# Optimization experiments

Hardware: AMD Instinct MI355X
Metric: run time of the kernel (lower is better)

The kernel has to match this reference:

```python
import jax, jax.numpy as jnp
import numpy as np

B, T, HID = 2, 2048, 2048
N_HEADS, N_KV, HEAD_DIM = 32, 8, 64
THETA = 10000.0
SCALE = HEAD_DIM ** -0.5
STEPS = 2  # entries already in cache before this call (step_idx)


def _rope_cos_sin(pos):
    # pos: [B, T] int -> cos/sin [B, T, HEAD_DIM]
    inv_freq = 1.0 / (THETA ** (jnp.arange(0, HEAD_DIM, 2, dtype=jnp.float32) / HEAD_DIM))
    freqs = pos.astype(jnp.float32)[..., None] * inv_freq  # [B,T,D/2]
    emb = jnp.concatenate([freqs, freqs], axis=-1)
    return jnp.cos(emb), jnp.sin(emb)


def _rotate_half(x):
    x1, x2 = jnp.split(x, 2, axis=-1)
    return jnp.concatenate([-x2, x1], axis=-1)


def setup_inputs() -> dict:
    key = jax.random.key(0)
    ks = jax.random.split(key, 8)
    combined_states = jax.random.normal(ks[0], (B, T, 2 * HID), dtype=jnp.float32)
    # additive causal mask: 0 on/below diagonal, large negative above
    causal = jnp.tril(jnp.ones((T, T), dtype=bool))
    attention_mask = jnp.where(causal, 0.0, -1e9).astype(jnp.float32)[None, None].repeat(B, axis=0)
    position_ids = jnp.broadcast_to(jnp.arange(T, dtype=jnp.int32), (B, T))
    prev_k = jax.random.normal(ks[1], (STEPS, B, N_HEADS, T, HEAD_DIM), dtype=jnp.float32)
    prev_v = jax.random.normal(ks[2], (STEPS, B, N_HEADS, T, HEAD_DIM), dtype=jnp.float32)
    Wq = 0.02 * jax.random.normal(ks[3], (2 * HID, N_HEADS * HEAD_DIM), dtype=jnp.float32)
    Wk = 0.02 * jax.random.normal(ks[4], (2 * HID, N_KV * HEAD_DIM), dtype=jnp.float32)
    Wv = 0.02 * jax.random.normal(ks[5], (2 * HID, N_KV * HEAD_DIM), dtype=jnp.float32)
    Wo = 0.02 * jax.random.normal(ks[6], (N_HEADS * HEAD_DIM, HID), dtype=jnp.float32)
    return {"combined_states": combined_states, "attention_mask": attention_mask,
            "position_ids": position_ids, "prev_k": prev_k, "prev_v": prev_v,
            "Wq": Wq, "Wk": Wk, "Wv": Wv, "Wo": Wo}


def reference(combined_states, attention_mask, position_ids, prev_k, prev_v, Wq, Wk, Wv, Wo):
    b, t, _ = combined_states.shape
    step_idx = prev_k.shape[0]  # len(cache_k) before append
    groups = N_HEADS // N_KV

    # fused QKV projection -> [B, H, T, D]
    q = (combined_states @ Wq).reshape(b, t, N_HEADS, HEAD_DIM).transpose(0, 2, 1, 3)
    k = (combined_states @ Wk).reshape(b, t, N_KV, HEAD_DIM).transpose(0, 2, 1, 3)
    v = (combined_states @ Wv).reshape(b, t, N_KV, HEAD_DIM).transpose(0, 2, 1, 3)

    # RoPE with phase shift by step_idx
    cos, sin = _rope_cos_sin(position_ids + step_idx)
    cos, sin = cos[:, None], sin[:, None]  # [B,1,T,D]
    q = q * cos + _rotate_half(q) * sin
    k = k * cos + _rotate_half(k) * sin

    # GQA expansion (repeat_interleave over head dim)
    k = jnp.repeat(k, groups, axis=1)
    v = jnp.repeat(v, groups, axis=1)

    # cache after append: [prev_0, prev_1, ..., k_new]; k0 = cache[0], later = cache[1:]
    k0, v0 = prev_k[0], prev_v[0]
    later_k = jnp.concatenate([prev_k[1:], k[None]], axis=0)  # [S, B, H, T, D], S = step_idx
    later_v = jnp.concatenate([prev_v[1:], v[None]], axis=0)

    # block attention over K_0 plus growing diagonal terms
    attn = jnp.einsum('bhtd,bhsd->bhts', q, k0) * SCALE + attention_mask  # [B,H,T,T]
    diag = jnp.einsum('bhtd,sbhtd->bhts', q, later_k) * SCALE             # [B,H,T,S]
    logits = jnp.concatenate([attn, diag], axis=-1)                        # [B,H,T,T+S]
    probs = jax.nn.softmax(logits.astype(jnp.float32), axis=-1).astype(q.dtype)

    out = jnp.einsum('bhts,bhsd->bhtd', probs[..., :t], v0)
    out = out + jnp.einsum('bhts,sbhtd->bhtd', probs[..., t:], later_v)
    out = out.transpose(0, 2, 1, 3).reshape(b, t, N_HEADS * HEAD_DIM)
    return out @ Wo
```

## Files before the change

kernel.cpp:

```cpp
#include <hip/hip_runtime.h>

#define B_    2
#define T_    2048
#define HID_  2048
#define NH_   32
#define NKV_  8
#define HD_   64
#define STEPS_ 2
#define SCALE_ 0.125f
#define CSC_  0.18033688011112042f

typedef float   f32x4  __attribute__((ext_vector_type(4)));
typedef __bf16  bf16x8 __attribute__((ext_vector_type(8)));
typedef unsigned short u16x8 __attribute__((ext_vector_type(8)));

__device__ __forceinline__ unsigned short f2bf(float f) {
  unsigned int u = __builtin_bit_cast(unsigned int, f);
  u = (u + 0x7fffu + ((u >> 16) & 1u)) >> 16;
  return (unsigned short)u;
}
__device__ __forceinline__ float bf2f(unsigned short h) {
  unsigned int u = ((unsigned int)h) << 16;
  return __builtin_bit_cast(float, u);
}
__device__ __forceinline__ bf16x8 frag_ld(const unsigned short* p) {
  u16x8 v = *(const u16x8*)p;
  return __builtin_bit_cast(bf16x8, v);
}
__device__ __forceinline__ f32x4 mfma16(bf16x8 a, bf16x8 b, f32x4 c) {
  return __builtin_amdgcn_mfma_f32_16x16x32_bf16(a, b, c, 0, 0, 0);
}
__device__ __forceinline__ void async_cp16(const void* g, void* l) {
  __builtin_amdgcn_global_load_lds(
      (const __attribute__((address_space(1))) void*)g,
      (__attribute__((address_space(3))) void*)l, 16, 0, 0);
}
__device__ __forceinline__ unsigned int cvtpk_bf16(float lo, float hi) {
  unsigned int r;
  asm("v_cvt_pk_bf16_f32 %0, %1, %2" : "=v"(r) : "v"(lo), "v"(hi));
  return r;
}

__global__ __launch_bounds__(256) void preproc(const float* __restrict__ X,
                                               const float* __restrict__ prevk,
                                               const float* __restrict__ prevv,
                                               const float* __restrict__ Wq,
                                               const float* __restrict__ Wk,
                                               const float* __restrict__ Wv,
                                               const float* __restrict__ Wo,
                                               const int* __restrict__ pos_ids,
                                               unsigned short* __restrict__ Xb,
                                               unsigned short* __restrict__ k0b,
                                               unsigned short* __restrict__ WqkvT,
                                               unsigned short* __restrict__ WoT,
                                               unsigned short* __restrict__ v0t,
                                               float2* __restrict__ cstab) {
  __shared__ float tile[128][65];
  const int tid = threadIdx.x;
  int blk = blockIdx.x;

  if (blk < 16384) {
    int idx = blk * 256 + tid;
    float4 v = ((const float4*)X)[idx];
    ushort4 o;
    o.x = f2bf(v.x); o.y = f2bf(v.y); o.z = f2bf(v.z); o.w = f2bf(v.w);
    ((ushort4*)Xb)[idx] = o;
    return;
  }
  blk -= 16384;
  if (blk < 8192) {
    int idx = blk * 256 + tid;
    float4 v = ((const float4*)prevk)[idx];
    ushort4 o;
    o.x = f2bf(v.x); o.y = f2bf(v.y); o.z = f2bf(v.z); o.w = f2bf(v.w);
    ((ushort4*)k0b)[idx] = o;
    return;
  }
  blk -= 8192;
  if (blk < 512) {
    int idx = blk * 256 + tid;
    int i = idx & 31;
    int pos = pos_ids[idx >> 5] + STEPS_;
    float inv = exp2f(-(float)i * (13.287712379549449f / 32.0f));
    float ang = (float)pos * inv;
    float ss, cc;
    sincosf(ang, &ss, &cc);
    cstab[idx] = make_float2(cc, ss);
    return;
  }
  blk -= 512;

  const float* in;
  unsigned short* out;
  int N, ldo, k0, n0;
  if (blk < 1536) {
    int nt = blk % 48, kt = blk / 48;
    k0 = kt * 128;
    ldo = 4096;
    if (nt < 32)      { in = Wq; N = 2048; out = WqkvT;                         n0 = nt * 64; }
    else if (nt < 40) { in = Wk; N = 512;  out = WqkvT + (size_t)2048 * 4096;   n0 = (nt - 32) * 64; }
    else              { in = Wv; N = 512;  out = WqkvT + (size_t)2560 * 4096;   n0 = (nt - 40) * 64; }
  } else if (blk < 2048) {
    int q = blk - 1536;
    int nt = q % 32, kt = q / 32;
    in = Wo; out = WoT; N = 2048; ldo = 2048;
    k0 = kt * 128; n0 = nt * 64;
  } else {
    int q = blk - 2048;
    int st = q % 16, bh = q / 16;
    in = prevv + (size_t)bh * T_ * HD_;
    out = v0t + (size_t)bh * HD_ * T_;
    N = 64; ldo = T_;
    k0 = st * 128; n0 = 0;
  }

  const int c = tid & 63, w = tid >> 6;
#pragma unroll
  for (int i = 0; i < 32; i++) {
    int r = w * 32 + i;
    tile[r][c] = in[(size_t)(k0 + r) * N + n0 + c];
  }
  __syncthreads();
#pragma unroll
  for (int ii = 0; ii < 16; ii++) {
    int rr = w * 16 + ii;
    unsigned int u = (unsigned int)f2bf(tile[c * 2][rr]) |
                     ((unsigned int)f2bf(tile[c * 2 + 1][rr]) << 16);
    *(unsigned int*)&out[(size_t)(n0 + rr) * ldo + k0 + c * 2] = u;
  }
}

#define SBAR  do { __builtin_amdgcn_sched_barrier(0); __builtin_amdgcn_s_barrier(); \
                   __builtin_amdgcn_sched_barrier(0); } while (0)
#define LGKM0 do { asm volatile("s_waitcnt lgkmcnt(0)" ::: "memory"); \
                   __builtin_amdgcn_sched_barrier(0); } while (0)
#define VM2   do { asm volatile("s_waitcnt vmcnt(2)" ::: "memory"); } while (0)
#define VM0   do { asm volatile("s_waitcnt vmcnt(0)" ::: "memory"); } while (0)

template <int NF>
__global__ __launch_bounds__(512, 2) void gemm128_bt(const unsigned short* __restrict__ A,
                                                     const unsigned short* __restrict__ Bt,
                                                     float* __restrict__ C,
                                                     int M, int N, int K) {
  constexpr int NHF = NF / 2;
  constexpr int BROWS = 128 + NF * 64;
  __shared__ __attribute__((aligned(128))) unsigned short smem[2][BROWS * 64];

  const int tid  = threadIdx.x;
  const int lane = tid & 63;
  const int wid  = tid >> 6;
  const int wr   = wid >> 2;
  const int wc   = wid & 3;
  const int la   = lane & 15;
  const int lq   = lane >> 4;
  const int sw   = la & 7;
  const int m0   = blockIdx.x * 128;
  const int n0   = blockIdx.y * (NF * 64);

  const int sr = lane >> 3;
  const int sl = (lane & 7) ^ sr;

  const unsigned short* gA[2];
  const unsigned short* gB[NHF][2];
#pragma unroll
  for (int is = 0; is < 2; ++is) {
    int r = (wid * 2 + is) * 8 + sr;
    gA[is] = A + (size_t)(m0 + r) * K + sl * 8;
#pragma unroll
    for (int u = 0; u < NHF; ++u)
      gB[u][is] = Bt + (size_t)(n0 + u * 128 + r) * K + sl * 8;
  }

#define G_STG_A(buf, kt) do { \
    async_cp16(gA[0] + (size_t)(kt) * 64, &smem[buf][(wid * 2 + 0) * 512]); \
    async_cp16(gA[1] + (size_t)(kt) * 64, &smem[buf][(wid * 2 + 1) * 512]); \
  } while (0)
#define G_STG_B(buf, u, kt) do { \
    async_cp16(gB[u][0] + (size_t)(kt) * 64, &smem[buf][(128 + (u) * 128) * 64 + (wid * 2 + 0) * 512]); \
    async_cp16(gB[u][1] + (size_t)(kt) * 64, &smem[buf][(128 + (u) * 128) * 64 + (wid * 2 + 1) * 512]); \
  } while (0)

  f32x4  acc[4][NF] = {};
  bf16x8 aR[2][2], b0r[NHF][2], b1r[NHF][2];

#define G_RD_A(buf, qm) do { \
    const unsigned short* rp_ = &smem[buf][0]; \
    _Pragma("unroll") \
    for (int i_ = 0; i_ < 2; ++i_) { \
      int ro_ = (wr * 64 + (qm) * 32 + i_ * 16 + la) * 64; \
      aR[i_][0] = frag_ld(rp_ + ro_ + (((0 + lq) ^ sw) << 3)); \
      aR[i_][1] = frag_ld(rp_ + ro_ + (((4 + lq) ^ sw) << 3)); \
    } \
  } while (0)
#define G_RD_B(buf, qn, breg) do { \
    const unsigned short* rp_ = &smem[buf][128 * 64]; \
    _Pragma("unroll") \
    for (int j_ = 0; j_ < NHF; ++j_) { \
      int ro_ = (wc * (NF * 16) + (qn) * (NF * 8) + j_ * 16 + la) * 64; \
      breg[j_][0] = frag_ld(rp_ + ro_ + (((0 + lq) ^ sw) << 3)); \
      breg[j_][1] = frag_ld(rp_ + ro_ + (((4 + lq) ^ sw) << 3)); \
    } \
  } while (0)
#define G_MMA(qm, qn, breg) do { \
    _Pragma("unroll") \
    for (int i_ = 0; i_ < 2; ++i_) \
      _Pragma("unroll") \
      for (int j_ = 0; j_ < NHF; ++j_) { \
        f32x4 c_ = acc[(qm) * 2 + i_][(qn) * NHF + j_]; \
        c_ = mfma16(aR[i_][0], breg[j_][0], c_); \
        c_ = mfma16(aR[i_][1], breg[j_][1], c_); \
        acc[(qm) * 2 + i_][(qn) * NHF + j_] = c_; \
      } \
  } while (0)

  G_STG_A(0, 0);
#pragma unroll
  for (int u = 0; u < NHF; ++u) G_STG_B(0, u, 0);
  if constexpr (NF == 6) G_STG_B(1, 2, 1); else G_STG_A(1, 1);
  VM2;
  SBAR;

  const int NI = K >> 7;
  for (int it = 0; it < NI; ++it) {
    const int e = it * 2;
    const bool pf = (it + 1 < NI);
    G_RD_A(0, 0);
    G_RD_B(0, 0, b0r);
    if constexpr (NF == 6) G_STG_A(1, e + 1); else G_STG_B(1, 0, e + 1);
    SBAR; LGKM0;
    __builtin_amdgcn_s_setprio(1); G_MMA(0, 0, b0r); __builtin_amdgcn_s_setprio(0);
    SBAR;
    G_RD_B(0, 1, b1r);
    if constexpr (NF == 6) G_STG_B(1, 0, e + 1); else G_STG_B(1, 1, e + 1);
    SBAR; LGKM0;
    __builtin_amdgcn_s_setprio(1); G_MMA(0, 1, b1r); __builtin_amdgcn_s_setprio(0);
    SBAR;
    G_RD_A(0, 1);
    if constexpr (NF == 6) G_STG_B(1, 1, e + 1);
    SBAR; LGKM0;
    __builtin_amdgcn_s_setprio(1); G_MMA(1, 1, b1r); __builtin_amdgcn_s_setprio(0);
    SBAR;
    if (pf) G_STG_A(0, e + 2);
    SBAR; LGKM0;
    __builtin_amdgcn_s_setprio(1); G_MMA(1, 0, b0r); __builtin_amdgcn_s_setprio(0);
    if (pf) { VM2; } else { VM0; }
    SBAR;
    G_RD_A(1, 0);
    G_RD_B(1, 0, b0r);
    if (pf) G_STG_B(0, 0, e + 2);
    SBAR; LGKM0;
    __builtin_amdgcn_s_setprio(1); G_MMA(0, 0, b0r); __builtin_amdgcn_s_setprio(0);
    SBAR;
    G_RD_B(1, 1, b1r);
    if (pf) G_STG_B(0, 1, e + 2);
    SBAR; LGKM0;
    __builtin_amdgcn_s_setprio(1); G_MMA(0, 1, b1r); __builtin_amdgcn_s_setprio(0);
    SBAR;
    G_RD_A(1, 1);
    if constexpr (NF == 6) { if (pf) G_STG_B(0, 2, e + 2); }
    SBAR; LGKM0;
    __builtin_amdgcn_s_setprio(1); G_MMA(1, 1, b1r); __builtin_amdgcn_s_setprio(0);
    SBAR;
    if constexpr (NF == 6) { if (pf) G_STG_B(1, 2, e + 3); }
    else                   { if (pf) G_STG_A(1, e + 3); }
    SBAR; LGKM0;
    __builtin_amdgcn_s_setprio(1); G_MMA(1, 0, b0r); __builtin_amdgcn_s_setprio(0);
    VM2;
    SBAR;
  }

#pragma unroll
  for (int mf = 0; mf < 4; ++mf) {
    int row = m0 + wr * 64 + mf * 16 + lq * 4;
#pragma unroll
    for (int nf = 0; nf < NF; ++nf) {
      int col = n0 + wc * (NF * 16) + nf * 16 + la;
#pragma unroll
      for (int r = 0; r < 4; ++r)
        C[(size_t)(row + r) * N + col] = acc[mf][nf][r];
    }
  }
#undef G_STG_A
#undef G_STG_B
#undef G_RD_A
#undef G_RD_B
#undef G_MMA
}

__global__ __launch_bounds__(256, 3) void flash_kernel(const float* __restrict__ QKV,
                                                       const unsigned short* __restrict__ k0b,
                                                       const unsigned short* __restrict__ v0t,
                                                       const float* __restrict__ prev_k,
                                                       const float* __restrict__ prev_v,
                                                       const float2* __restrict__ cstab,
                                                       unsigned short* __restrict__ attnout) {
  __shared__ unsigned short sK[2][64 * 64];
  __shared__ unsigned short sV[2][64 * 64];
  __shared__ unsigned short sP[4][2][16 * 72];

  const int tid = threadIdx.x;
  const int lane = tid & 63;
  const int wave = tid >> 6;
  const int la = lane & 15;
  const int lq = lane >> 4;
  const int swz = la & 7;

  const int id = blockIdx.x;
  const int bh = (id & 7) * 8 + ((id >> 3) & 7);
  const int qt = 15 - (id >> 6);

  const size_t bhs = (size_t)bh;
  const unsigned short* gK = k0b + bhs * T_ * HD_;
  const unsigned short* gV = v0t + bhs * HD_ * T_;

  const int rb0 = qt * 128 + wave * 32;
  const int ktd = rb0 >> 6;
  const int ktmax = 2 * qt + 1;

  const int bI = bh >> 5;
  const int hI = bh & 31;
  const int kvI = hI >> 2;

  const int lrow = lane >> 3;
  const int lcb = (lane & 7) ^ lrow;

  {
    unsigned short* kd = &sK[0][wave * 1024];
    unsigned short* vd = &sV[0][wave * 1024];
    async_cp16(gK + (size_t)(wave * 16 + lrow) * HD_ + lcb * 8, kd);
    async_cp16(gK + (size_t)(wave * 16 + 8 + lrow) * HD_ + lcb * 8, kd + 512);
    async_cp16(gV + (size_t)(wave * 16 + lrow) * T_ + lcb * 8, vd);
    async_cp16(gV + (size_t)(wave * 16 + 8 + lrow) * T_ + lcb * 8, vd + 512);
  }

  bf16x8 aq[2][2];
#pragma unroll
  for (int f = 0; f < 2; f++) {
    const int t = rb0 + f * 16 + la;
    const float* qrow = QKV + ((size_t)(bI * T_ + t)) * 3072 + hI * 64;
    const float2* ct = cstab + (size_t)(bI * T_ + t) * 32 + lq * 8;
    u16x8 a0, a1;
#pragma unroll
    for (int j = 0; j < 8; j++) {
      int i = lq * 8 + j;
      float2 cs = ct[j];
      float x1 = qrow[i];
      float x2 = qrow[32 + i];
      a0[j] = f2bf((x1 * cs.x - x2 * cs.y) * CSC_);
      a1[j] = f2bf((x2 * cs.x + x1 * cs.y) * CSC_);
    }
    aq[f][0] = __builtin_bit_cast(bf16x8, a0);
    aq[f][1] = __builtin_bit_cast(bf16x8, a1);
  }

  f32x4 o[2][4] = {};
  float m_f[2] = {-1e30f, -1e30f};
  float l_p[2] = {0.0f, 0.0f};

  __syncthreads();

  int cur = 0;
  for (int kt = 0; kt <= ktmax; ++kt) {
    if (kt < ktmax) {
      const int nk = (kt + 1) * 64;
      unsigned short* kd = &sK[cur ^ 1][wave * 1024];
      unsigned short* vd = &sV[cur ^ 1][wave * 1024];
      async_cp16(gK + (size_t)(nk + wave * 16 + lrow) * HD_ + lcb * 8, kd);
      async_cp16(gK + (size_t)(nk + wave * 16 + 8 + lrow) * HD_ + lcb * 8, kd + 512);
      async_cp16(gV + (size_t)(wave * 16 + lrow) * T_ + nk + lcb * 8, vd);
      async_cp16(gV + (size_t)(wave * 16 + 8 + lrow) * T_ + nk + lcb * 8, vd + 512);
    }

    if (kt <= ktd) {
      const unsigned short* kb = &sK[cur][0];
      const unsigned short* vb = &sV[cur][0];

      bf16x8 bk0[4], bk1[4];
#pragma unroll
      for (int nb = 0; nb < 4; nb++) {
        const unsigned short* rp = kb + (nb * 16 + la) * 64;
        bk0[nb] = frag_ld(rp + ((lq ^ swz) << 3));
        bk1[nb] = frag_ld(rp + (((lq + 4) ^ swz) << 3));
      }
      f32x4 s[2][4];
      __builtin_amdgcn_s_setprio(1);
#pragma unroll
      for (int f = 0; f < 2; f++)
#pragma unroll
        for (int nb = 0; nb < 4; nb++) {
          f32x4 z = {0.f, 0.f, 0.f, 0.f};
          z = mfma16(bk0[nb], aq[f][0], z);
          z = mfma16(bk1[nb], aq[f][1], z);
          s[f][nb] = z;
        }
      __builtin_amdgcn_s_setprio(0);

      bf16x8 bv0[4], bv1[4];
#pragma unroll
      for (int jd = 0; jd < 4; jd++) {
        const unsigned short* rp = vb + (jd * 16 + la) * 64;
        bv0[jd] = frag_ld(rp + ((lq ^ swz) << 3));
        bv1[jd] = frag_ld(rp + (((lq + 4) ^ swz) << 3));
      }

      const bool diag = (kt == ktd);
#pragma unroll
      for (int f = 0; f < 2; f++) {
        const int qrow = rb0 + f * 16 + la;
        if (diag) {
#pragma unroll
          for (int nb = 0; nb < 4; nb++)
#pragma unroll
            for (int r = 0; r < 4; r++) {
              int key = kt * 64 + nb * 16 + lq * 4 + r;
              s[f][nb][r] = (key <= qrow) ? s[f][nb][r] : -1e30f;
            }
        }
        float t0 = fmaxf(fmaxf(s[f][0][0], s[f][0][1]), fmaxf(s[f][0][2], s[f][0][3]));
        float t1 = fmaxf(fmaxf(s[f][1][0], s[f][1][1]), fmaxf(s[f][1][2], s[f][1][3]));
        float t2 = fmaxf(fmaxf(s[f][2][0], s[f][2][1]), fmaxf(s[f][2][2], s[f][2][3]));
        float t3 = fmaxf(fmaxf(s[f][3][0], s[f][3][1]), fmaxf(s[f][3][2], s[f][3][3]));
        float tm = fmaxf(fmaxf(t0, t1), fmaxf(t2, t3));
        const bool resc = __any(tm > m_f[f] + 8.0f);
        if (resc) {
          tm = fmaxf(tm, __shfl_xor(tm, 16));
          tm = fmaxf(tm, __shfl_xor(tm, 32));
          float mn = fmaxf(m_f[f], tm);
          float al = exp2f(m_f[f] - mn);
          m_f[f] = mn;
          l_p[f] *= al;
          float a0 = __shfl(al, lq * 4 + 0);
          float a1 = __shfl(al, lq * 4 + 1);
          float a2 = __shfl(al, lq * 4 + 2);
          float a3 = __shfl(al, lq * 4 + 3);
#pragma unroll
          for (int jd = 0; jd < 4; jd++) {
            o[f][jd][0] *= a0;
            o[f][jd][1] *= a1;
            o[f][jd][2] *= a2;
            o[f][jd][3] *= a3;
          }
        }
        float ls = 0.0f;
#pragma unroll
        for (int nb = 0; nb < 4; nb++)
#pragma unroll
          for (int r = 0; r < 4; r++) {
            float p = exp2f(s[f][nb][r] - m_f[f]);
            s[f][nb][r] = p;
            ls += p;
          }
        l_p[f] += ls;
        unsigned short* pw = &sP[wave][f][0];
#pragma unroll
        for (int nb = 0; nb < 4; nb++) {
          unsigned int p01 = cvtpk_bf16(s[f][nb][0], s[f][nb][1]);
          unsigned int p23 = cvtpk_bf16(s[f][nb][2], s[f][nb][3]);
          unsigned long long pq = ((unsigned long long)p23 << 32) | (unsigned long long)p01;
          *(unsigned long long*)(pw + la * 72 + nb * 16 + lq * 4) = pq;
        }
      }

#pragma unroll
      for (int f = 0; f < 2; f++) {
        const unsigned short* pr = &sP[wave][f][0];
        bf16x8 ap0 = frag_ld(&pr[la * 72 + lq * 8]);
        bf16x8 ap1 = frag_ld(&pr[la * 72 + 32 + lq * 8]);
        __builtin_amdgcn_s_setprio(1);
#pragma unroll
        for (int jd = 0; jd < 4; jd++) {
          o[f][jd] = mfma16(ap0, bv0[jd], o[f][jd]);
          o[f][jd] = mfma16(ap1, bv1[jd], o[f][jd]);
        }
        __builtin_amdgcn_s_setprio(0);
      }
    }
    __syncthreads();
    cur ^= 1;
  }

#pragma unroll
  for (int f = 0; f < 2; f++) {
    l_p[f] += __shfl_xor(l_p[f], 16);
    l_p[f] += __shfl_xor(l_p[f], 32);
  }

  const size_t P1 = (size_t)B_ * NH_ * T_ * HD_;
  const float* k1base = prev_k + P1 + bhs * T_ * HD_;
  const float* v1base = prev_v + P1 + bhs * T_ * HD_;
  const float* vnbase = QKV + (size_t)bI * T_ * 3072 + 2560 + kvI * 64;
  unsigned short* aobase = attnout + (size_t)bI * T_ * (NH_ * HD_) + hI * HD_;

#pragma unroll
  for (int f = 0; f < 2; f++) {
    const int rowA = rb0 + f * 16 + la;
    const float* k1p = k1base + (size_t)rowA * HD_;
    const float* krow = QKV + ((size_t)(bI * T_ + rowA)) * 3072 + 2048 + kvI * 64;
    const float2* ct = cstab + (size_t)(bI * T_ + rowA) * 32 + lq * 8;
    float e1 = 0.f, e2 = 0.f;
#pragma unroll
    for (int h2 = 0; h2 < 2; h2++) {
      const int dd = h2 * 32 + lq * 8;
#pragma unroll
      for (int j = 0; j < 8; j++) {
        float qv = (h2 == 0) ? (float)aq[f][0][j] : (float)aq[f][1][j];
        e1 = fmaf(qv, k1p[dd + j], e1);
      }
    }
#pragma unroll
    for (int j = 0; j < 8; j++) {
      int i = lq * 8 + j;
      float2 cs = ct[j];
      float x1 = krow[i];
      float x2 = krow[32 + i];
      e2 = fmaf((float)aq[f][0][j], x1 * cs.x - x2 * cs.y, e2);
      e2 = fmaf((float)aq[f][1][j], x2 * cs.x + x1 * cs.y, e2);
    }
    e1 += __shfl_xor(e1, 16); e1 += __shfl_xor(e1, 32);
    e2 += __shfl_xor(e2, 16); e2 += __shfl_xor(e2, 32);
    float mx = fmaxf(m_f[f], fmaxf(e1, e2));
    float w0 = exp2f(m_f[f] - mx);
    float w1 = exp2f(e1 - mx);
    float w2 = exp2f(e2 - mx);
    float inv = 1.0f / (l_p[f] * w0 + w1 + w2);
    float s0 = w0 * inv, s1 = w1 * inv, s2 = w2 * inv;
    float a0[4], a1[4], a2[4];
#pragma unroll
    for (int r = 0; r < 4; r++) {
      a0[r] = __shfl(s0, lq * 4 + r);
      a1[r] = __shfl(s1, lq * 4 + r);
      a2[r] = __shfl(s2, lq * 4 + r);
    }
#pragma unroll
    for (int r = 0; r < 4; r++) {
      const int rowO = rb0 + f * 16 + lq * 4 + r;
      const float* v1p = v1base + (size_t)rowO * HD_;
      const float* vnp = vnbase + (size_t)rowO * 3072;
      unsigned short* aop = aobase + (size_t)rowO * (NH_ * HD_);
#pragma unroll
      for (int jd = 0; jd < 4; jd++) {
        int d = jd * 16 + la;
        float out = o[f][jd][r] * a0[r] + v1p[d] * a1[r] + vnp[d] * a2[r];
        aop[d] = f2bf(out);
      }
    }
  }
}

#define OFF_QKV   ((size_t)0)
#define OFF_XB    ((size_t)50331648)
#define OFF_WQKVT ((size_t)83886080)
#define OFF_WOT   ((size_t)109051904)
#define OFF_K0B   ((size_t)134217728)
#define OFF_V0T   ((size_t)150994944)
#define OFF_CS    ((size_t)167772160)

extern "C" void kernel_launch(void* const* d_in, const int* in_sizes, int n_in,
                              void* d_out, int out_size, void* d_ws, size_t ws_size,
                              hipStream_t stream) {
  const float* X = (const float*)d_in[0];
  const int* pos = (const int*)d_in[2];
  const float* prevk = (const float*)d_in[3];
  const float* prevv = (const float*)d_in[4];
  const float* Wq = (const float*)d_in[5];
  const float* Wk = (const float*)d_in[6];
  const float* Wv = (const float*)d_in[7];
  const float* Wo = (const float*)d_in[8];

  char* ws = (char*)d_ws;
  float* QKV = (float*)(ws + OFF_QKV);
  unsigned short* Xb = (unsigned short*)(ws + OFF_XB);
  unsigned short* WqkvT = (unsigned short*)(ws + OFF_WQKVT);
  unsigned short* attnout = (unsigned short*)(ws + OFF_WQKVT);
  unsigned short* WoT = (unsigned short*)(ws + OFF_WOT);
  unsigned short* k0b = (unsigned short*)(ws + OFF_K0B);
  unsigned short* v0t = (unsigned short*)(ws + OFF_V0T);
  float2* cstab = (float2*)(ws + OFF_CS);

  preproc<<<28160, 256, 0, stream>>>(X, prevk, prevv, Wq, Wk, Wv, Wo, pos,
                                     Xb, k0b, WqkvT, WoT, v0t, cstab);

  gemm128_bt<6><<<dim3(32, 8), 512, 0, stream>>>(Xb, WqkvT, QKV, 4096, 3072, 4096);

  flash_kernel<<<1024, 256, 0, stream>>>(QKV, k0b, v0t, prevk, prevv, cstab, attnout);

  gemm128_bt<4><<<dim3(32, 8), 512, 0, stream>>>(attnout, WoT, (float*)d_out, 4096, 2048, 2048);
}
```

Measured before the change: 468.3 us.

## Restructure GEMM main loop into four phases with whole-B-tile prefetch

Reorganizes the bf16 GEMM software pipeline. Each half-iteration now issues both B fragment reads up front and runs two MMA groups per phase, which halves the number of workgroup barriers per K step. All B sub-tiles are staged with one grouped async copy, and the vmcnt waits are retuned to 4 or 6 to match the new issue order. The trade-offs are fewer points where staging can interleave with MFMA work, higher register pressure from keeping both B fragment sets live, and tighter ordering assumptions in the async-copy wait counts.

```diff
diff --git a/kernel.cpp b/kernel.cpp
--- a/kernel.cpp
+++ b/kernel.cpp
@@ -134,7 +134,8 @@
                    __builtin_amdgcn_sched_barrier(0); } while (0)
 #define LGKM0 do { asm volatile("s_waitcnt lgkmcnt(0)" ::: "memory"); \
                    __builtin_amdgcn_sched_barrier(0); } while (0)
-#define VM2   do { asm volatile("s_waitcnt vmcnt(2)" ::: "memory"); } while (0)
+#define VM4   do { asm volatile("s_waitcnt vmcnt(4)" ::: "memory"); } while (0)
+#define VM6   do { asm volatile("s_waitcnt vmcnt(6)" ::: "memory"); } while (0)
 #define VM0   do { asm volatile("s_waitcnt vmcnt(0)" ::: "memory"); } while (0)
 
 template <int NF>
@@ -178,6 +179,10 @@
 #define G_STG_B(buf, u, kt) do { \
     async_cp16(gB[u][0] + (size_t)(kt) * 64, &smem[buf][(128 + (u) * 128) * 64 + (wid * 2 + 0) * 512]); \
     async_cp16(gB[u][1] + (size_t)(kt) * 64, &smem[buf][(128 + (u) * 128) * 64 + (wid * 2 + 1) * 512]); \
+  } while (0)
+#define G_STG_BALL(buf, kt) do { \
+    _Pragma("unroll") \
+    for (int u_ = 0; u_ < NHF; ++u_) G_STG_B(buf, u_, kt); \
   } while (0)
 
   f32x4  acc[4][NF] = {};
@@ -212,12 +217,12 @@
         acc[(qm) * 2 + i_][(qn) * NHF + j_] = c_; \
       } \
   } while (0)
+#define VMN do { if constexpr (NF == 6) { VM6; } else { VM4; } } while (0)
 
   G_STG_A(0, 0);
-#pragma unroll
-  for (int u = 0; u < NHF; ++u) G_STG_B(0, u, 0);
-  if constexpr (NF == 6) G_STG_B(1, 2, 1); else G_STG_A(1, 1);
-  VM2;
+  G_STG_BALL(0, 0);
+  G_STG_BALL(1, 1);
+  VMN;
   SBAR;
 
   const int NI = K >> 7;
@@ -226,46 +231,37 @@
     const bool pf = (it + 1 < NI);
     G_RD_A(0, 0);
     G_RD_B(0, 0, b0r);
-    if constexpr (NF == 6) G_STG_A(1, e + 1); else G_STG_B(1, 0, e + 1);
+    G_RD_B(0, 1, b1r);
+    G_STG_A(1, e + 1);
     SBAR; LGKM0;
-    __builtin_amdgcn_s_setprio(1); G_MMA(0, 0, b0r); __builtin_amdgcn_s_setprio(0);
-    SBAR;
-    G_RD_B(0, 1, b1r);
-    if constexpr (NF == 6) G_STG_B(1, 0, e + 1); else G_STG_B(1, 1, e + 1);
-    SBAR; LGKM0;
-    __builtin_amdgcn_s_setprio(1); G_MMA(0, 1, b1r); __builtin_amdgcn_s_setprio(0);
+    __builtin_amdgcn_s_setprio(1);
+    G_MMA(0, 0, b0r); G_MMA(0, 1, b1r);
+    __builtin_amdgcn_s_setprio(0);
     SBAR;
     G_RD_A(0, 1);
-    if constexpr (NF == 6) G_STG_B(1, 1, e + 1);
+    if (pf) G_STG_BALL(0, e + 2);
     SBAR; LGKM0;
-    __builtin_amdgcn_s_setprio(1); G_MMA(1, 1, b1r); __builtin_amdgcn_s_setprio(0);
-    SBAR;
-    if (pf) G_STG_A(0, e + 2);
-    SBAR; LGKM0;
-    __builtin_amdgcn_s_setprio(1); G_MMA(1, 0, b0r); __builtin_amdgcn_s_setprio(0);
-    if (pf) { VM2; } else { VM0; }
+    __builtin_amdgcn_s_setprio(1);
+    G_MMA(1, 1, b1r); G_MMA(1, 0, b0r);
+    __builtin_amdgcn_s_setprio(0);
+    if (pf) { VMN; } else { VM0; }
     SBAR;
     G_RD_A(1, 0);
     G_RD_B(1, 0, b0r);
-    if (pf) G_STG_B(0, 0, e + 2);
+    G_RD_B(1, 1, b1r);
+    if (pf) G_STG_A(0, e + 2);
     SBAR; LGKM0;
-    __builtin_amdgcn_s_setprio(1); G_MMA(0, 0, b0r); __builtin_amdgcn_s_setprio(0);
-    SBAR;
-    G_RD_B(1, 1, b1r);
-    if (pf) G_STG_B(0, 1, e + 2);
-    SBAR; LGKM0;
-    __builtin_amdgcn_s_setprio(1); G_MMA(0, 1, b1r); __builtin_amdgcn_s_setprio(0);
+    __builtin_amdgcn_s_setprio(1);
+    G_MMA(0, 0, b0r); G_MMA(0, 1, b1r);
+    __builtin_amdgcn_s_setprio(0);
     SBAR;
     G_RD_A(1, 1);
-    if constexpr (NF == 6) { if (pf) G_STG_B(0, 2, e + 2); }
+    if (pf) G_STG_BALL(1, e + 3);
     SBAR; LGKM0;
-    __builtin_amdgcn_s_setprio(1); G_MMA(1, 1, b1r); __builtin_amdgcn_s_setprio(0);
-    SBAR;
-    if constexpr (NF == 6) { if (pf) G_STG_B(1, 2, e + 3); }
-    else                   { if (pf) G_STG_A(1, e + 3); }
-    SBAR; LGKM0;
-    __builtin_amdgcn_s_setprio(1); G_MMA(1, 0, b0r); __builtin_amdgcn_s_setprio(0);
-    VM2;
+    __builtin_amdgcn_s_setprio(1);
+    G_MMA(1, 1, b1r); G_MMA(1, 0, b0r);
+    __builtin_amdgcn_s_setprio(0);
+    VMN;
     SBAR;
   }
 
@@ -282,9 +278,11 @@
   }
 #undef G_STG_A
 #undef G_STG_B
+#undef G_STG_BALL
 #undef G_RD_A
 #undef G_RD_B
 #undef G_MMA
+#undef VMN
 }
 
 __global__ __launch_bounds__(256, 3) void flash_kernel(const float* __restrict__ QKV,
```

New measurement: 474.8 us. No clear change (+1.4%).
